# Performance work log

Measured on AMD Instinct MI355X. Metric: run time of the kernel, lower is better.

Reference implementation:

```python
import jax, jax.numpy as jnp
import numpy as np

NB, B, T, D, H = 7, 16, 512, 128, 2
HD = D // H

def _ln(x, s, b):
    m = jnp.mean(x, -1, keepdims=True)
    v = jnp.mean((x - m) ** 2, -1, keepdims=True)
    return (x - m) * jax.lax.rsqrt(v + 1e-5) * s + b

def setup_inputs():
    key = jax.random.key(0)
    keys = iter(jax.random.split(key, 80))
    def w(*shape):
        return jax.random.normal(next(keys), shape, jnp.float32) * 0.02
    inp = {}
    inp['bands'] = jax.random.normal(next(keys), (NB, B, T, D), jnp.float32)
    for nm in ['Wq', 'Wk', 'Wv', 'Wo']:
        inp[nm] = w(NB, D, D)
    for nm in ['bq', 'bk', 'bv', 'bo']:
        inp[nm] = jnp.zeros((NB, D), jnp.float32)
    inp['g_ls'] = jnp.ones((3, D), jnp.float32); inp['g_lb'] = jnp.zeros((3, D), jnp.float32)
    inp['g_w1'] = w(3, D, 2 * D); inp['g_b1'] = jnp.zeros((3, 2 * D), jnp.float32)
    inp['g_w2'] = w(3, 2 * D, D); inp['g_b2'] = jnp.zeros((3, D), jnp.float32)
    inp['g_wg'] = w(3, D, D);     inp['g_bg'] = jnp.zeros((3, D), jnp.float32)
    inp['h_ls'] = jnp.ones((2, D), jnp.float32); inp['h_lb'] = jnp.zeros((2, D), jnp.float32)
    inp['h_w1'] = w(2, D, 3 * D); inp['h_b1'] = jnp.zeros((2, 3 * D), jnp.float32)
    inp['h_w2'] = w(2, 3 * D, D); inp['h_b2'] = jnp.zeros((2, D), jnp.float32)
    inp['r_ls'] = jnp.ones((2, D), jnp.float32); inp['r_lb'] = jnp.zeros((2, D), jnp.float32)
    inp['r_w1'] = w(2, D, 4 * D); inp['r_b1'] = jnp.zeros((2, 4 * D), jnp.float32)
    inp['r_w2'] = w(2, 4 * D, D); inp['r_b2'] = jnp.zeros((2, D), jnp.float32)
    # wormhole: pairs (0,6),(1,5),(2,4) share cross_proj per pair; bridge on band 3
    inp['wp_w'] = w(3, D, D);     inp['wp_b'] = jnp.zeros((3, D), jnp.float32)
    inp['wg_w'] = w(3, 2 * D, D); inp['wg_b'] = jnp.zeros((3, D), jnp.float32)
    inp['br_w'] = w(6, D, D);     inp['br_b'] = jnp.zeros((6, D), jnp.float32)
    inp['bg_w'] = w(2 * D, D);    inp['bg_b'] = jnp.zeros((D,), jnp.float32)
    return inp

def reference(bands, Wq, bq, Wk, bk, Wv, bv, Wo, bo,
              g_ls, g_lb, g_w1, g_b1, g_w2, g_b2, g_wg, g_bg,
              h_ls, h_lb, h_w1, h_b1, h_w2, h_b2,
              r_ls, r_lb, r_w1, r_b1, r_w2, r_b2,
              wp_w, wp_b, wg_w, wg_b, br_w, br_b, bg_w, bg_b):
    n, b, t, d = bands.shape
    # --- per-band causal self-attention, vectorized over the 7 bands ---
    def heads(x):  # [n,b,t,d] -> [n,b,H,t,hd]
        return x.reshape(n, b, t, H, HD).transpose(0, 1, 3, 2, 4)
    q = heads(jnp.einsum('nbtd,nde->nbte', bands, Wq) + bq[:, None, None, :])
    k = heads(jnp.einsum('nbtd,nde->nbte', bands, Wk) + bk[:, None, None, :])
    v = heads(jnp.einsum('nbtd,nde->nbte', bands, Wv) + bv[:, None, None, :])
    scores = jnp.einsum('nbhtd,nbhsd->nbhts', q, k) / np.float32(np.sqrt(HD))
    causal = jnp.triu(jnp.ones((t, t), bool), 1)
    scores = jnp.where(causal, jnp.float32(-1e9), scores)
    attn = jax.nn.softmax(scores, axis=-1)
    o = jnp.einsum('nbhts,nbhsd->nbhtd', attn, v)
    o = o.transpose(0, 1, 3, 2, 4).reshape(n, b, t, d)
    o = jnp.einsum('nbtd,nde->nbte', o, Wo) + bo[:, None, None, :]
    x = bands + o
    # --- band-tier FFN processors ---
    geo, hyb, rea = x[0:3], x[3:5], x[5:7]
    hg = _ln(geo, g_ls[:, None, None, :], g_lb[:, None, None, :])
    hg = jax.nn.gelu(jnp.einsum('nbtd,nde->nbte', hg, g_w1) + g_b1[:, None, None, :], approximate=False)
    hg = jnp.einsum('nbte,ned->nbtd', hg, g_w2) + g_b2[:, None, None, :]
    gate = jax.nn.sigmoid(jnp.einsum('nbtd,nde->nbte', geo, g_wg) + g_bg[:, None, None, :])
    geo = geo + gate * hg
    hh = _ln(hyb, h_ls[:, None, None, :], h_lb[:, None, None, :])
    hh = jax.nn.gelu(jnp.einsum('nbtd,nde->nbte', hh, h_w1) + h_b1[:, None, None, :], approximate=False)
    hyb = hyb + jnp.einsum('nbte,ned->nbtd', hh, h_w2) + h_b2[:, None, None, :]
    hr = _ln(rea, r_ls[:, None, None, :], r_lb[:, None, None, :])
    hr = jax.nn.gelu(jnp.einsum('nbtd,nde->nbte', hr, r_w1) + r_b1[:, None, None, :], approximate=False)
    rea = rea + jnp.einsum('nbte,ned->nbtd', hr, r_w2) + r_b2[:, None, None, :]
    y = jnp.concatenate([geo, hyb, rea], axis=0)
    # --- position-wise wormhole: pairs (0,6),(1,5),(2,4) + bridge band 3 ---
    bl = y[jnp.array([0, 1, 2])]   # low bands of each pair
    bh = y[jnp.array([6, 5, 4])]   # matching high bands
    info_lo = jnp.einsum('nbtd,nde->nbte', bh, wp_w) + wp_b[:, None, None, :]
    info_hi = jnp.einsum('nbtd,nde->nbte', bl, wp_w) + wp_b[:, None, None, :]
    gate_lo = jax.nn.sigmoid(jnp.einsum('nbtd,nde->nbte', jnp.concatenate([bl, info_lo], -1), wg_w) + wg_b[:, None, None, :])
    gate_hi = jax.nn.sigmoid(jnp.einsum('nbtd,nde->nbte', jnp.concatenate([bh, info_hi], -1), wg_w) + wg_b[:, None, None, :])
    out_lo = bl + gate_lo * info_lo
    out_hi = bh + gate_hi * info_hi
    others = y[jnp.array([0, 1, 2, 4, 5, 6])]
    bridge_info = (jnp.einsum('nbtd,nde->bte', others, br_w) + jnp.sum(br_b, 0)) / 6.0
    gate_br = jax.nn.sigmoid(jnp.concatenate([y[3], bridge_info], -1) @ bg_w + bg_b)
    out3 = y[3] + gate_br * bridge_info
    return jnp.stack([out_lo[0], out_lo[1], out_lo[2], out3, out_hi[2], out_hi[1], out_hi[0]], axis=0)
```

## Files before the change

### kernel.cpp

```cpp
#include <hip/hip_runtime.h>
#include <hip/hip_bf16.h>

#define NBAND 7
#define BBATCH 16
#define TSEQ 512
#define DMODEL 128
#define MBAND (BBATCH * TSEQ)
#define BANDE ((size_t)MBAND * DMODEL)

typedef __attribute__((ext_vector_type(8))) short short8;
typedef __attribute__((ext_vector_type(4))) float f32x4;
typedef unsigned int u32;
typedef unsigned short u16;

__device__ __forceinline__ u16 f2bf(float x) {
  unsigned u = __float_as_uint(x);
  unsigned r = u + 0x7FFF + ((u >> 16) & 1);
  return (u16)(r >> 16);
}
__device__ __forceinline__ u32 pack2(float a, float b) {
  return (u32)f2bf(a) | ((u32)f2bf(b) << 16);
}
__device__ __forceinline__ float b2f(u16 h) {
  return __uint_as_float((u32)h << 16);
}

struct TSlice { const float* src; u16* dst; int K, N; };
struct TArgs { TSlice s[62]; };

__global__ __launch_bounds__(256) void wtrans_kernel(TArgs a) {
  TSlice sl = a.s[blockIdx.z];
  const int tk = (blockIdx.x & 7) * 64, tn = (blockIdx.x >> 3) * 64;
  if (tk >= sl.K || tn >= sl.N) return;
  __shared__ __align__(16) u16 T[64][72];
  const int tid = threadIdx.x;
  #pragma unroll
  for (int it = 0; it < 4; ++it) {
    int idx = tid + it * 256;
    int k = idx >> 4, nq = (idx & 15) << 2;
    float4 v = *(const float4*)&sl.src[(size_t)(tk + k) * sl.N + tn + nq];
    T[nq + 0][k] = f2bf(v.x); T[nq + 1][k] = f2bf(v.y);
    T[nq + 2][k] = f2bf(v.z); T[nq + 3][k] = f2bf(v.w);
  }
  __syncthreads();
  #pragma unroll
  for (int it = 0; it < 2; ++it) {
    int idx = tid + it * 256;
    int n = idx >> 3, kq = (idx & 7) << 3;
    *(short8*)&sl.dst[(size_t)(tn + n) * sl.K + tk + kq] = *(const short8*)&T[n][kq];
  }
}

__device__ __forceinline__ void mfma_part_h(const u16* __restrict__ A,
                                            const u16* __restrict__ WT,
                                            int K, int m0, int n0, int tid,
                                            u16 (*As)[40], u16 (*Bs)[40],
                                            f32x4 acc[2][2]) {
  const int lane = tid & 63;
  const int wv = tid >> 6;
  const int wr = wv >> 1, wc = wv & 1;
  const int lr = lane & 15, k8 = lane >> 4;
  const int row = tid >> 2, kq = (tid & 3) << 3;

  const u16* Ar = &A[(size_t)(m0 + row) * K + kq];
  const u16* Br = &WT[(size_t)(n0 + row) * K + kq];
  short8 apre = *(const short8*)Ar;
  short8 bpre = *(const short8*)Br;

  for (int k0 = 0; k0 < K; k0 += 32) {
    __syncthreads();
    *(short8*)&As[row][kq] = apre;
    *(short8*)&Bs[row][kq] = bpre;
    if (k0 + 32 < K) {
      apre = *(const short8*)(Ar + k0 + 32);
      bpre = *(const short8*)(Br + k0 + 32);
    }
    __syncthreads();
    short8 a0 = *(const short8*)&As[wr * 32 + lr][k8 * 8];
    short8 a1 = *(const short8*)&As[wr * 32 + 16 + lr][k8 * 8];
    short8 b0 = *(const short8*)&Bs[wc * 32 + lr][k8 * 8];
    short8 b1 = *(const short8*)&Bs[wc * 32 + 16 + lr][k8 * 8];
    acc[0][0] = __builtin_amdgcn_mfma_f32_16x16x32_bf16(a0, b0, acc[0][0], 0, 0, 0);
    acc[0][1] = __builtin_amdgcn_mfma_f32_16x16x32_bf16(a0, b1, acc[0][1], 0, 0, 0);
    acc[1][0] = __builtin_amdgcn_mfma_f32_16x16x32_bf16(a1, b0, acc[1][0], 0, 0, 0);
    acc[1][1] = __builtin_amdgcn_mfma_f32_16x16x32_bf16(a1, b1, acc[1][1], 0, 0, 0);
  }
}

__device__ __forceinline__ void mfma_part_f(const float* __restrict__ A,
                                            const u16* __restrict__ WT,
                                            int K, int m0, int n0, int tid,
                                            u16 (*As)[40], u16 (*Bs)[40],
                                            f32x4 acc[2][2]) {
  const int lane = tid & 63;
  const int wv = tid >> 6;
  const int wr = wv >> 1, wc = wv & 1;
  const int lr = lane & 15, k8 = lane >> 4;
  const int row = tid >> 2, kq = (tid & 3) << 3;

  const float* Ar = &A[(size_t)(m0 + row) * K + kq];
  const u16* Br = &WT[(size_t)(n0 + row) * K + kq];
  float4 ap0 = *(const float4*)Ar;
  float4 ap1 = *(const float4*)(Ar + 4);
  short8 bpre = *(const short8*)Br;

  for (int k0 = 0; k0 < K; k0 += 32) {
    __syncthreads();
    *(u32*)&As[row][kq]     = pack2(ap0.x, ap0.y);
    *(u32*)&As[row][kq + 2] = pack2(ap0.z, ap0.w);
    *(u32*)&As[row][kq + 4] = pack2(ap1.x, ap1.y);
    *(u32*)&As[row][kq + 6] = pack2(ap1.z, ap1.w);
    *(short8*)&Bs[row][kq] = bpre;
    if (k0 + 32 < K) {
      ap0 = *(const float4*)(Ar + k0 + 32);
      ap1 = *(const float4*)(Ar + k0 + 36);
      bpre = *(const short8*)(Br + k0 + 32);
    }
    __syncthreads();
    short8 a0 = *(const short8*)&As[wr * 32 + lr][k8 * 8];
    short8 a1 = *(const short8*)&As[wr * 32 + 16 + lr][k8 * 8];
    short8 b0 = *(const short8*)&Bs[wc * 32 + lr][k8 * 8];
    short8 b1 = *(const short8*)&Bs[wc * 32 + 16 + lr][k8 * 8];
    acc[0][0] = __builtin_amdgcn_mfma_f32_16x16x32_bf16(a0, b0, acc[0][0], 0, 0, 0);
    acc[0][1] = __builtin_amdgcn_mfma_f32_16x16x32_bf16(a0, b1, acc[0][1], 0, 0, 0);
    acc[1][0] = __builtin_amdgcn_mfma_f32_16x16x32_bf16(a1, b0, acc[1][0], 0, 0, 0);
    acc[1][1] = __builtin_amdgcn_mfma_f32_16x16x32_bf16(a1, b1, acc[1][1], 0, 0, 0);
  }
}

struct ZD {
  const u16 *A, *A2, *WT, *WT2;
  const float* AF;
  const float* bias;
  const float* residF;
  const u16 *residH, *extraH;
  float* OF;
  u16* OH;
  int K, N, op;
  int pad;
};
struct PArgs { ZD z[21]; };

__global__ __launch_bounds__(256) void gemm_b(PArgs p) {
  const ZD d = p.z[blockIdx.z];
  const int n0 = blockIdx.y * 64;
  if (n0 >= d.N) return;
  __shared__ __align__(16) u16 As[64][40];
  __shared__ __align__(16) u16 Bs[64][40];
  const int m0 = blockIdx.x * 64;
  const int tid = threadIdx.x;
  f32x4 acc[2][2] = {};

  if (d.op == 7) {
    const int bl[6] = {0, 1, 2, 4, 5, 6};
    #pragma unroll 1
    for (int s = 0; s < 6; ++s)
      mfma_part_h(d.A + (size_t)bl[s] * BANDE, d.WT + (size_t)s * 16384,
                  128, m0, n0, tid, As, Bs, acc);
  } else {
    if (d.AF) mfma_part_f(d.AF, d.WT, d.K, m0, n0, tid, As, Bs, acc);
    else      mfma_part_h(d.A,  d.WT, d.K, m0, n0, tid, As, Bs, acc);
    if (d.A2)
      mfma_part_h(d.A2, d.WT2, d.K, m0, n0, tid, As, Bs, acc);
  }

  const int lane = tid & 63;
  const int wv = tid >> 6;
  const int wr = wv >> 1, wc = wv & 1;
  const int lr = lane & 15, lg = lane >> 4;

  if (d.op == 6) {
    #pragma unroll
    for (int i = 0; i < 2; ++i) {
      #pragma unroll
      for (int j = 0; j < 2; ++j) {
        int mb = m0 + wr * 32 + i * 16 + lg * 4;
        int n = n0 + wc * 32 + j * 16 + lr;
        float bia = d.bias[n];
        uint2 st;
        st.x = pack2(acc[i][j][0] + bia, acc[i][j][1] + bia);
        st.y = pack2(acc[i][j][2] + bia, acc[i][j][3] + bia);
        *(uint2*)&d.OH[(size_t)n * MBAND + mb] = st;
      }
    }
    return;
  }

  #pragma unroll
  for (int i = 0; i < 2; ++i) {
    #pragma unroll
    for (int j = 0; j < 2; ++j) {
      #pragma unroll
      for (int r = 0; r < 4; ++r) {
        int m = m0 + wr * 32 + i * 16 + lg * 4 + r;
        int n = n0 + wc * 32 + j * 16 + lr;
        float v = acc[i][j][r];
        if (d.bias && d.op != 7) v += d.bias[n];
        size_t idx = (size_t)m * d.N + n;
        switch (d.op) {
          case 0: d.OH[idx] = f2bf(v); break;
          case 1: d.OH[idx] =
                    f2bf(0.5f * v * (1.f + erff(v * 0.70710678118654752f))); break;
          case 2: d.OH[idx] = f2bf(1.f / (1.f + __expf(-v))); break;
          case 3: d.OH[idx] = f2bf(d.residF[idx] + v); break;
          case 4: {
            float gate = 1.f / (1.f + __expf(-v));
            d.OF[idx] = b2f(d.residH[idx]) + gate * b2f(d.extraH[idx]);
          } break;
          case 5: {
            float gm = d.extraH ? b2f(d.extraH[idx]) : 1.f;
            d.OH[idx] = f2bf(b2f(d.residH[idx]) + gm * v);
          } break;
          case 7: {
            float bb = 0.f;
            #pragma unroll
            for (int s = 0; s < 6; ++s) bb += d.bias[s * 128 + n];
            d.OH[idx] = f2bf(v * (1.f / 6.f) + bb * (1.f / 6.f));
          } break;
        }
      }
    }
  }
}

__global__ __launch_bounds__(256) void attn_kernel(const u16* __restrict__ q,
                                                   const u16* __restrict__ k,
                                                   const u16* __restrict__ vT,
                                                   u16* __restrict__ o) {
  const int band = blockIdx.x >> 8;
  const int rest = blockIdx.x & 255;
  const int qt = 7 - (rest & 7);
  const int bh = rest >> 3;
  const int h  = bh & 1;
  const int b  = bh >> 1;
  const size_t rowbase = ((size_t)band * BBATCH + b) * TSEQ;
  const u16* vb = vT + (size_t)band * BANDE + (size_t)h * 64 * MBAND + (size_t)b * TSEQ;

  const int tid  = threadIdx.x;
  const int w    = tid >> 6;
  const int lane = tid & 63;
  const int lr   = lane & 15;
  const int lg   = lane >> 4;

  __shared__ __align__(16) u16 Ks[64][72];
  __shared__ __align__(16) u16 Vs[64][72];
  __shared__ __align__(16) u16 Ps[4][16][72];

  short8 aq[2];
  {
    const u16* qp = &q[(rowbase + qt * 64 + w * 16 + lr) * DMODEL + h * 64 + lg * 8];
    aq[0] = *(const short8*)qp;
    aq[1] = *(const short8*)(qp + 32);
  }

  short8 kpre[2], vpre[2];
  #pragma unroll
  for (int it = 0; it < 2; ++it) {
    int idx = tid + it * 256;
    int r = idx >> 3, c8 = (idx & 7) << 3;
    kpre[it] = *(const short8*)&k[(rowbase + r) * DMODEL + h * 64 + c8];
    vpre[it] = *(const short8*)&vb[(size_t)r * MBAND + c8];
  }

  f32x4 oacc[4] = {};
  float m[4], l[4];
  #pragma unroll
  for (int r = 0; r < 4; ++r) { m[r] = -1e30f; l[r] = 0.f; }

  for (int kt = 0; kt <= qt; ++kt) {
    __syncthreads();
    #pragma unroll
    for (int it = 0; it < 2; ++it) {
      int idx = tid + it * 256;
      int r = idx >> 3, c8 = (idx & 7) << 3;
      *(short8*)&Ks[r][c8] = kpre[it];
      *(short8*)&Vs[r][c8] = vpre[it];
    }
    if (kt < qt) {
      int nt = kt + 1;
      #pragma unroll
      for (int it = 0; it < 2; ++it) {
        int idx = tid + it * 256;
        int r = idx >> 3, c8 = (idx & 7) << 3;
        kpre[it] = *(const short8*)&k[(rowbase + nt * 64 + r) * DMODEL + h * 64 + c8];
        vpre[it] = *(const short8*)&vb[(size_t)r * MBAND + nt * 64 + c8];
      }
    }
    __syncthreads();

    f32x4 s[4] = {};
    #pragma unroll
    for (int c = 0; c < 2; ++c) {
      short8 a = aq[c];
      #pragma unroll
      for (int j = 0; j < 4; ++j) {
        short8 bb = *(const short8*)&Ks[j * 16 + lr][c * 32 + lg * 8];
        s[j] = __builtin_amdgcn_mfma_f32_16x16x32_bf16(a, bb, s[j], 0, 0, 0);
      }
    }
    #pragma unroll
    for (int j = 0; j < 4; ++j)
      #pragma unroll
      for (int r = 0; r < 4; ++r)
        s[j][r] *= 0.125f;

    if (kt == qt) {
      #pragma unroll
      for (int j = 0; j < 4; ++j)
        #pragma unroll
        for (int r = 0; r < 4; ++r) {
          int row = w * 16 + lg * 4 + r;
          int col = j * 16 + lr;
          if (col > row) s[j][r] = -1e30f;
        }
    }

    float mx[4], al[4];
    #pragma unroll
    for (int r = 0; r < 4; ++r)
      mx[r] = fmaxf(fmaxf(s[0][r], s[1][r]), fmaxf(s[2][r], s[3][r]));
    #pragma unroll
    for (int off = 1; off <= 8; off <<= 1)
      #pragma unroll
      for (int r = 0; r < 4; ++r)
        mx[r] = fmaxf(mx[r], __shfl_xor(mx[r], off));
    #pragma unroll
    for (int r = 0; r < 4; ++r) {
      float mn = fmaxf(m[r], mx[r]);
      al[r] = __expf(m[r] - mn);
      m[r] = mn;
    }
    float rs[4] = {0.f, 0.f, 0.f, 0.f};
    #pragma unroll
    for (int j = 0; j < 4; ++j)
      #pragma unroll
      for (int r = 0; r < 4; ++r) {
        float pe = __expf(s[j][r] - m[r]);
        s[j][r] = pe;
        rs[r] += pe;
      }
    #pragma unroll
    for (int off = 1; off <= 8; off <<= 1)
      #pragma unroll
      for (int r = 0; r < 4; ++r)
        rs[r] += __shfl_xor(rs[r], off);
    #pragma unroll
    for (int r = 0; r < 4; ++r) l[r] = l[r] * al[r] + rs[r];

    #pragma unroll
    for (int j = 0; j < 4; ++j)
      #pragma unroll
      for (int r = 0; r < 4; ++r)
        oacc[j][r] *= al[r];

    #pragma unroll
    for (int j = 0; j < 4; ++j)
      #pragma unroll
      for (int r = 0; r < 4; ++r)
        Ps[w][lg * 4 + r][j * 16 + lr] = f2bf(s[j][r]);

    #pragma unroll
    for (int c = 0; c < 2; ++c) {
      short8 a = *(const short8*)&Ps[w][lr][c * 32 + lg * 8];
      #pragma unroll
      for (int j = 0; j < 4; ++j) {
        short8 bb = *(const short8*)&Vs[j * 16 + lr][c * 32 + lg * 8];
        oacc[j] = __builtin_amdgcn_mfma_f32_16x16x32_bf16(a, bb, oacc[j], 0, 0, 0);
      }
    }
  }

  float inv[4];
  #pragma unroll
  for (int r = 0; r < 4; ++r) inv[r] = 1.f / l[r];
  #pragma unroll
  for (int j = 0; j < 4; ++j)
    #pragma unroll
    for (int r = 0; r < 4; ++r) {
      size_t row = rowbase + qt * 64 + w * 16 + lg * 4 + r;
      o[row * DMODEL + h * 64 + j * 16 + lr] = f2bf(oacc[j][r] * inv[r]);
    }
}

struct LNA {
  const u16* x;
  u16* xn;
  const float* ls[7];
  const float* lb[7];
};

__global__ __launch_bounds__(256) void ln_kernel(LNA p) {
  const int tid = threadIdx.x;
  const int rr = tid >> 6, lane = tid & 63;
  const size_t row = (size_t)blockIdx.x * 4 + rr;
  u32 wv = *(const u32*)&p.x[row * DMODEL + 2 * lane];
  float a = b2f((u16)wv), b = b2f((u16)(wv >> 16));
  float s = a + b;
  #pragma unroll
  for (int off = 32; off; off >>= 1) s += __shfl_xor(s, off);
  float mean = s * (1.f / 128.f);
  float da = a - mean, db = b - mean;
  float vs = da * da + db * db;
  #pragma unroll
  for (int off = 32; off; off >>= 1) vs += __shfl_xor(vs, off);
  float rstd = rsqrtf(vs * (1.f / 128.f) + 1e-5f);
  int band = (int)(row >> 13);
  const float* ls = p.ls[band];
  const float* lb = p.lb[band];
  *(u32*)&p.xn[row * DMODEL + 2 * lane] =
      pack2(da * rstd * ls[2 * lane] + lb[2 * lane],
            db * rstd * ls[2 * lane + 1] + lb[2 * lane + 1]);
}

extern "C" void kernel_launch(void* const* d_in, const int* in_sizes, int n_in,
                              void* d_out, int out_size, void* d_ws, size_t ws_size,
                              hipStream_t stream) {
  bool dict = (in_sizes[2] != 896);
  const float* bands = (const float*)d_in[0];
  const float* Wq = (const float*)d_in[1];
  const float *Wk, *Wv, *Wo, *bq, *bk, *bv, *bo;
  if (dict) {
    Wk = (const float*)d_in[2]; Wv = (const float*)d_in[3]; Wo = (const float*)d_in[4];
    bq = (const float*)d_in[5]; bk = (const float*)d_in[6];
    bv = (const float*)d_in[7]; bo = (const float*)d_in[8];
  } else {
    bq = (const float*)d_in[2]; Wk = (const float*)d_in[3]; bk = (const float*)d_in[4];
    Wv = (const float*)d_in[5]; bv = (const float*)d_in[6];
    Wo = (const float*)d_in[7]; bo = (const float*)d_in[8];
  }
  const float* g_ls = (const float*)d_in[9];
  const float* g_lb = (const float*)d_in[10];
  const float* g_w1 = (const float*)d_in[11];
  const float* g_b1 = (const float*)d_in[12];
  const float* g_w2 = (const float*)d_in[13];
  const float* g_b2 = (const float*)d_in[14];
  const float* g_wg = (const float*)d_in[15];
  const float* g_bg = (const float*)d_in[16];
  const float* h_ls = (const float*)d_in[17];
  const float* h_lb = (const float*)d_in[18];
  const float* h_w1 = (const float*)d_in[19];
  const float* h_b1 = (const float*)d_in[20];
  const float* h_w2 = (const float*)d_in[21];
  const float* h_b2 = (const float*)d_in[22];
  const float* r_ls = (const float*)d_in[23];
  const float* r_lb = (const float*)d_in[24];
  const float* r_w1 = (const float*)d_in[25];
  const float* r_b1 = (const float*)d_in[26];
  const float* r_w2 = (const float*)d_in[27];
  const float* r_b2 = (const float*)d_in[28];
  const float* wp_w = (const float*)d_in[29];
  const float* wp_b = (const float*)d_in[30];
  const float* wg_w = (const float*)d_in[31];
  const float* wg_b = (const float*)d_in[32];
  const float* br_w = (const float*)d_in[33];
  const float* br_b = (const float*)d_in[34];
  const float* bg_w = (const float*)d_in[35];
  const float* bg_b = (const float*)d_in[36];
  float* out = (float*)d_out;

  const float* lsP[7] = {g_ls, g_ls + 128, g_ls + 256, h_ls, h_ls + 128, r_ls, r_ls + 128};
  const float* lbP[7] = {g_lb, g_lb + 128, g_lb + 256, h_lb, h_lb + 128, r_lb, r_lb + 128};
  const float* b1p[7] = {g_b1, g_b1 + 256, g_b1 + 512,
                         h_b1, h_b1 + 384, r_b1, r_b1 + 512};
  const float* b2p[7] = {g_b2, g_b2 + 128, g_b2 + 256,
                         h_b2, h_b2 + 128, r_b2, r_b2 + 128};
  const int hN[7] = {256, 256, 256, 384, 384, 512, 512};

  const size_t HIDSZ = (size_t)MBAND * 2560;
  u16* H = (u16*)d_ws;
  u16* hidh = H;
  u16* qh = H + HIDSZ;
  u16* kh = qh + 7 * BANDE;
  u16* vh = kh + 7 * BANDE;
  u16* oh = vh + 7 * BANDE;
  u16* wt = oh + 7 * BANDE;
  u16* wtQ   = wt;
  u16* wtK   = wtQ + 7 * 16384;
  u16* wtV   = wtK + 7 * 16384;
  u16* wtO   = wtV + 7 * 16384;
  u16* wtGwg = wtO + 7 * 16384;
  u16* wtWp  = wtGwg + 3 * 16384;
  u16* wtBr  = wtWp + 3 * 16384;
  u16* wtWg  = wtBr + 6 * 16384;
  u16* wtBg  = wtWg + 6 * 16384;
  u16* wtG1  = wtBg + 2 * 16384;
  u16* wtH1  = wtG1 + 3 * 32768;
  u16* wtR1  = wtH1 + 2 * 49152;
  u16* wtG2  = wtR1 + 2 * 65536;
  u16* wtH2  = wtG2 + 3 * 32768;
  u16* wtR2  = wtH2 + 2 * 49152;
  u16* xh = qh;
  u16* xnh = kh;
  u16* gateh = vh;
  u16* yh = oh;
  u16* infoh = hidh;
  u16* bridgeh = hidh + 6 * BANDE;

  size_t hOff[7];
  {
    size_t acc = 0;
    for (int n = 0; n < 7; ++n) { hOff[n] = acc; acc += (size_t)MBAND * hN[n]; }
  }
  u16* wtW1s[7] = {wtG1, wtG1 + 32768, wtG1 + 65536,
                   wtH1, wtH1 + 49152, wtR1, wtR1 + 65536};
  u16* wtW2s[7] = {wtG2, wtG2 + 32768, wtG2 + 65536,
                   wtH2, wtH2 + 49152, wtR2, wtR2 + 65536};

  auto LP = [&](PArgs& p, int Z, int ymax) {
    dim3 grid(MBAND / 64, ymax, Z);
    gemm_b<<<grid, dim3(256), 0, stream>>>(p);
  };

  {
    TArgs ta{};
    int ns = 0;
    auto add = [&](const float* s, u16* d, int K, int N) {
      ta.s[ns].src = s; ta.s[ns].dst = d; ta.s[ns].K = K; ta.s[ns].N = N; ++ns;
    };
    for (int z = 0; z < 7; ++z) add(Wq + z * 16384, wtQ + z * 16384, 128, 128);
    for (int z = 0; z < 7; ++z) add(Wk + z * 16384, wtK + z * 16384, 128, 128);
    for (int z = 0; z < 7; ++z) add(Wv + z * 16384, wtV + z * 16384, 128, 128);
    for (int z = 0; z < 7; ++z) add(Wo + z * 16384, wtO + z * 16384, 128, 128);
    for (int i = 0; i < 3; ++i) add(g_wg + i * 16384, wtGwg + i * 16384, 128, 128);
    for (int i = 0; i < 3; ++i) add(wp_w + i * 16384, wtWp + i * 16384, 128, 128);
    for (int j = 0; j < 6; ++j) add(br_w + j * 16384, wtBr + j * 16384, 128, 128);
    for (int i = 0; i < 3; ++i) {
      add(wg_w + i * 32768,         wtWg + (size_t)(2 * i) * 16384,     128, 128);
      add(wg_w + i * 32768 + 16384, wtWg + (size_t)(2 * i + 1) * 16384, 128, 128);
    }
    add(bg_w,         wtBg,         128, 128);
    add(bg_w + 16384, wtBg + 16384, 128, 128);
    for (int i = 0; i < 3; ++i) add(g_w1 + i * 32768, wtG1 + i * 32768, 128, 256);
    for (int i = 0; i < 2; ++i) add(h_w1 + i * 49152, wtH1 + i * 49152, 128, 384);
    for (int i = 0; i < 2; ++i) add(r_w1 + i * 65536, wtR1 + i * 65536, 128, 512);
    for (int i = 0; i < 3; ++i) add(g_w2 + i * 32768, wtG2 + i * 32768, 256, 128);
    for (int i = 0; i < 2; ++i) add(h_w2 + i * 49152, wtH2 + i * 49152, 384, 128);
    for (int i = 0; i < 2; ++i) add(r_w2 + i * 65536, wtR2 + i * 65536, 512, 128);
    wtrans_kernel<<<dim3(64, 1, 62), dim3(256), 0, stream>>>(ta);
  }

  {
    PArgs p{};
    const u16* wtQKV[3] = {wtQ, wtK, wtV};
    const float* bqkv[3] = {bq, bk, bv};
    u16* oqkv[3] = {qh, kh, vh};
    for (int w = 0; w < 3; ++w)
      for (int band = 0; band < 7; ++band) {
        ZD& d = p.z[w * 7 + band];
        d.AF = bands + (size_t)band * BANDE;
        d.WT = wtQKV[w] + (size_t)band * 16384;
        d.bias = bqkv[w] + band * 128;
        d.OH = oqkv[w] + (size_t)band * BANDE;
        d.K = 128; d.N = 128; d.op = (w == 2) ? 6 : 0;
      }
    LP(p, 21, 2);
  }

  attn_kernel<<<dim3(NBAND * 256), dim3(256), 0, stream>>>(qh, kh, vh, oh);

  {
    PArgs p{};
    for (int band = 0; band < 7; ++band) {
      ZD& d = p.z[band];
      d.A = oh + (size_t)band * BANDE;
      d.WT = wtO + (size_t)band * 16384;
      d.bias = bo + band * 128;
      d.residF = bands + (size_t)band * BANDE;
      d.OH = xh + (size_t)band * BANDE;
      d.K = 128; d.N = 128; d.op = 3;
    }
    LP(p, 7, 2);
  }

  {
    LNA p{};
    p.x = xh; p.xn = xnh;
    for (int n = 0; n < 7; ++n) { p.ls[n] = lsP[n]; p.lb[n] = lbP[n]; }
    ln_kernel<<<dim3(NBAND * MBAND / 4), dim3(256), 0, stream>>>(p);
  }

  {
    PArgs p{};
    for (int z = 0; z < 3; ++z) {
      ZD& d = p.z[z];
      d.A = xh + (size_t)z * BANDE;
      d.WT = wtGwg + (size_t)z * 16384;
      d.bias = g_bg + z * 128;
      d.OH = gateh + (size_t)z * BANDE;
      d.K = 128; d.N = 128; d.op = 2;
    }
    for (int band = 0; band < 7; ++band) {
      ZD& d = p.z[3 + band];
      d.A = xnh + (size_t)band * BANDE;
      d.WT = wtW1s[band];
      d.bias = b1p[band];
      d.OH = hidh + hOff[band];
      d.K = 128; d.N = hN[band]; d.op = 1;
    }
    LP(p, 10, 8);
  }

  {
    PArgs p{};
    for (int band = 0; band < 7; ++band) {
      ZD& d = p.z[band];
      d.A = hidh + hOff[band];
      d.WT = wtW2s[band];
      d.bias = b2p[band];
      d.residH = xh + (size_t)band * BANDE;
      d.extraH = (band < 3) ? gateh + (size_t)band * BANDE : nullptr;
      d.OH = yh + (size_t)band * BANDE;
      d.K = hN[band]; d.N = 128; d.op = 5;
    }
    LP(p, 7, 2);
  }

  {
    PArgs p{};
    for (int z = 0; z < 6; ++z) {
      int t = (z < 3) ? z : z + 1;
      int src = 6 - t;
      int i = (t < 3) ? t : 6 - t;
      ZD& d = p.z[z];
      d.A = yh + (size_t)src * BANDE;
      d.WT = wtWp + (size_t)i * 16384;
      d.bias = wp_b + i * 128;
      d.OH = infoh + (size_t)z * BANDE;
      d.K = 128; d.N = 128; d.op = 0;
    }
    {
      ZD& d = p.z[6];
      d.A = yh;
      d.WT = wtBr;
      d.bias = br_b;
      d.OH = bridgeh;
      d.K = 128; d.N = 128; d.op = 7;
    }
    LP(p, 7, 2);
  }

  {
    PArgs p{};
    for (int z = 0; z < 6; ++z) {
      int t = (z < 3) ? z : z + 1;
      int i = (t < 3) ? t : 6 - t;
      ZD& d = p.z[z];
      d.A = yh + (size_t)t * BANDE;
      d.WT = wtWg + (size_t)(2 * i) * 16384;
      d.A2 = infoh + (size_t)z * BANDE;
      d.WT2 = wtWg + (size_t)(2 * i + 1) * 16384;
      d.bias = wg_b + i * 128;
      d.residH = yh + (size_t)t * BANDE;
      d.extraH = infoh + (size_t)z * BANDE;
      d.OF = out + (size_t)t * BANDE;
      d.K = 128; d.N = 128; d.op = 4;
    }
    {
      ZD& d = p.z[6];
      d.A = yh + 3 * BANDE;
      d.WT = wtBg;
      d.A2 = bridgeh;
      d.WT2 = wtBg + 16384;
      d.bias = bg_b;
      d.residH = yh + 3 * BANDE;
      d.extraH = bridgeh;
      d.OF = out + 3 * BANDE;
      d.K = 128; d.N = 128; d.op = 4;
    }
    LP(p, 7, 2);
  }
}
```

Baseline: 220.4 us.

## Pair causal query tiles per block to balance attention work and share K/V loads

The attention kernel now launches 512-thread blocks, each handling two query tiles (qt = 7-p and qt = p) with four waves apiece. Every block then does a fixed eight tiles of causal work, and the two tiles share each K/V tile staged in shared memory. This removes the load imbalance of triangular causal blocks and halves redundant K/V loads. In exchange, the waves on the shorter tile sit idle at barriers during later iterations, and the larger blocks may lower occupancy.

```diff
diff --git a/kernel.cpp b/kernel.cpp
--- a/kernel.cpp
+++ b/kernel.cpp
@@ -223,16 +223,15 @@
   }
 }
 
-__global__ __launch_bounds__(256) void attn_kernel(const u16* __restrict__ q,
+__global__ __launch_bounds__(512) void attn_kernel(const u16* __restrict__ q,
                                                    const u16* __restrict__ k,
                                                    const u16* __restrict__ vT,
                                                    u16* __restrict__ o) {
-  const int band = blockIdx.x >> 8;
-  const int rest = blockIdx.x & 255;
-  const int qt = 7 - (rest & 7);
-  const int bh = rest >> 3;
-  const int h  = bh & 1;
-  const int b  = bh >> 1;
+  const int bx   = blockIdx.x;
+  const int pp   = bx & 3;
+  const int h    = (bx >> 2) & 1;
+  const int b    = (bx >> 3) & 15;
+  const int band = bx >> 7;
   const size_t rowbase = ((size_t)band * BBATCH + b) * TSEQ;
   const u16* vb = vT + (size_t)band * BANDE + (size_t)h * 64 * MBAND + (size_t)b * TSEQ;
 
@@ -242,130 +241,121 @@
   const int lr   = lane & 15;
   const int lg   = lane >> 4;
 
+  const int qtA = 7 - pp;
+  const int qt_w = (w < 4) ? qtA : pp;
+  const int wr4 = w & 3;
+
   __shared__ __align__(16) u16 Ks[64][72];
   __shared__ __align__(16) u16 Vs[64][72];
-  __shared__ __align__(16) u16 Ps[4][16][72];
+  __shared__ __align__(16) u16 Ps[8][16][72];
 
   short8 aq[2];
   {
-    const u16* qp = &q[(rowbase + qt * 64 + w * 16 + lr) * DMODEL + h * 64 + lg * 8];
+    const u16* qp = &q[(rowbase + qt_w * 64 + wr4 * 16 + lr) * DMODEL + h * 64 + lg * 8];
     aq[0] = *(const short8*)qp;
     aq[1] = *(const short8*)(qp + 32);
   }
 
-  short8 kpre[2], vpre[2];
-  #pragma unroll
-  for (int it = 0; it < 2; ++it) {
-    int idx = tid + it * 256;
-    int r = idx >> 3, c8 = (idx & 7) << 3;
-    kpre[it] = *(const short8*)&k[(rowbase + r) * DMODEL + h * 64 + c8];
-    vpre[it] = *(const short8*)&vb[(size_t)r * MBAND + c8];
-  }
+  const int sr = tid >> 3, sc8 = (tid & 7) << 3;
+  short8 kpre = *(const short8*)&k[(rowbase + sr) * DMODEL + h * 64 + sc8];
+  short8 vpre = *(const short8*)&vb[(size_t)sr * MBAND + sc8];
 
   f32x4 oacc[4] = {};
   float m[4], l[4];
   #pragma unroll
   for (int r = 0; r < 4; ++r) { m[r] = -1e30f; l[r] = 0.f; }
 
-  for (int kt = 0; kt <= qt; ++kt) {
+  for (int kt = 0; kt <= qtA; ++kt) {
     __syncthreads();
-    #pragma unroll
-    for (int it = 0; it < 2; ++it) {
-      int idx = tid + it * 256;
-      int r = idx >> 3, c8 = (idx & 7) << 3;
-      *(short8*)&Ks[r][c8] = kpre[it];
-      *(short8*)&Vs[r][c8] = vpre[it];
-    }
-    if (kt < qt) {
+    *(short8*)&Ks[sr][sc8] = kpre;
+    *(short8*)&Vs[sr][sc8] = vpre;
+    if (kt < qtA) {
       int nt = kt + 1;
-      #pragma unroll
-      for (int it = 0; it < 2; ++it) {
-        int idx = tid + it * 256;
-        int r = idx >> 3, c8 = (idx & 7) << 3;
-        kpre[it] = *(const short8*)&k[(rowbase + nt * 64 + r) * DMODEL + h * 64 + c8];
-        vpre[it] = *(const short8*)&vb[(size_t)r * MBAND + nt * 64 + c8];
+      kpre = *(const short8*)&k[(rowbase + nt * 64 + sr) * DMODEL + h * 64 + sc8];
+      vpre = *(const short8*)&vb[(size_t)sr * MBAND + nt * 64 + sc8];
+    }
+    __syncthreads();
+
+    if (kt <= qt_w) {
+      f32x4 s[4] = {};
+      #pragma unroll
+      for (int c = 0; c < 2; ++c) {
+        short8 a = aq[c];
+        #pragma unroll
+        for (int j = 0; j < 4; ++j) {
+          short8 bb = *(const short8*)&Ks[j * 16 + lr][c * 32 + lg * 8];
+          s[j] = __builtin_amdgcn_mfma_f32_16x16x32_bf16(a, bb, s[j], 0, 0, 0);
+        }
       }
-    }
-    __syncthreads();
-
-    f32x4 s[4] = {};
-    #pragma unroll
-    for (int c = 0; c < 2; ++c) {
-      short8 a = aq[c];
-      #pragma unroll
-      for (int j = 0; j < 4; ++j) {
-        short8 bb = *(const short8*)&Ks[j * 16 + lr][c * 32 + lg * 8];
-        s[j] = __builtin_amdgcn_mfma_f32_16x16x32_bf16(a, bb, s[j], 0, 0, 0);
+      #pragma unroll
+      for (int j = 0; j < 4; ++j)
+        #pragma unroll
+        for (int r = 0; r < 4; ++r)
+          s[j][r] *= 0.125f;
+
+      if (kt == qt_w) {
+        #pragma unroll
+        for (int j = 0; j < 4; ++j)
+          #pragma unroll
+          for (int r = 0; r < 4; ++r) {
+            int row = wr4 * 16 + lg * 4 + r;
+            int col = j * 16 + lr;
+            if (col > row) s[j][r] = -1e30f;
+          }
       }
-    }
-    #pragma unroll
-    for (int j = 0; j < 4; ++j)
+
+      float mx[4], al[4];
       #pragma unroll
       for (int r = 0; r < 4; ++r)
-        s[j][r] *= 0.125f;
-
-    if (kt == qt) {
+        mx[r] = fmaxf(fmaxf(s[0][r], s[1][r]), fmaxf(s[2][r], s[3][r]));
+      #pragma unroll
+      for (int off = 1; off <= 8; off <<= 1)
+        #pragma unroll
+        for (int r = 0; r < 4; ++r)
+          mx[r] = fmaxf(mx[r], __shfl_xor(mx[r], off));
+      #pragma unroll
+      for (int r = 0; r < 4; ++r) {
+        float mn = fmaxf(m[r], mx[r]);
+        al[r] = __expf(m[r] - mn);
+        m[r] = mn;
+      }
+      float rs[4] = {0.f, 0.f, 0.f, 0.f};
       #pragma unroll
       for (int j = 0; j < 4; ++j)
         #pragma unroll
         for (int r = 0; r < 4; ++r) {
-          int row = w * 16 + lg * 4 + r;
-          int col = j * 16 + lr;
-          if (col > row) s[j][r] = -1e30f;
+          float pe = __expf(s[j][r] - m[r]);
+          s[j][r] = pe;
+          rs[r] += pe;
         }
-    }
-
-    float mx[4], al[4];
-    #pragma unroll
-    for (int r = 0; r < 4; ++r)
-      mx[r] = fmaxf(fmaxf(s[0][r], s[1][r]), fmaxf(s[2][r], s[3][r]));
-    #pragma unroll
-    for (int off = 1; off <= 8; off <<= 1)
-      #pragma unroll
-      for (int r = 0; r < 4; ++r)
-        mx[r] = fmaxf(mx[r], __shfl_xor(mx[r], off));
-    #pragma unroll
-    for (int r = 0; r < 4; ++r) {
-      float mn = fmaxf(m[r], mx[r]);
-      al[r] = __expf(m[r] - mn);
-      m[r] = mn;
-    }
-    float rs[4] = {0.f, 0.f, 0.f, 0.f};
-    #pragma unroll
-    for (int j = 0; j < 4; ++j)
-      #pragma unroll
-      for (int r = 0; r < 4; ++r) {
-        float pe = __expf(s[j][r] - m[r]);
-        s[j][r] = pe;
-        rs[r] += pe;
-      }
-    #pragma unroll
-    for (int off = 1; off <= 8; off <<= 1)
-      #pragma unroll
-      for (int r = 0; r < 4; ++r)
-        rs[r] += __shfl_xor(rs[r], off);
-    #pragma unroll
-    for (int r = 0; r < 4; ++r) l[r] = l[r] * al[r] + rs[r];
-
-    #pragma unroll
-    for (int j = 0; j < 4; ++j)
-      #pragma unroll
-      for (int r = 0; r < 4; ++r)
-        oacc[j][r] *= al[r];
-
-    #pragma unroll
-    for (int j = 0; j < 4; ++j)
-      #pragma unroll
-      for (int r = 0; r < 4; ++r)
-        Ps[w][lg * 4 + r][j * 16 + lr] = f2bf(s[j][r]);
-
-    #pragma unroll
-    for (int c = 0; c < 2; ++c) {
-      short8 a = *(const short8*)&Ps[w][lr][c * 32 + lg * 8];
-      #pragma unroll
-      for (int j = 0; j < 4; ++j) {
-        short8 bb = *(const short8*)&Vs[j * 16 + lr][c * 32 + lg * 8];
-        oacc[j] = __builtin_amdgcn_mfma_f32_16x16x32_bf16(a, bb, oacc[j], 0, 0, 0);
+      #pragma unroll
+      for (int off = 1; off <= 8; off <<= 1)
+        #pragma unroll
+        for (int r = 0; r < 4; ++r)
+          rs[r] += __shfl_xor(rs[r], off);
+      #pragma unroll
+      for (int r = 0; r < 4; ++r) l[r] = l[r] * al[r] + rs[r];
+
+      #pragma unroll
+      for (int j = 0; j < 4; ++j)
+        #pragma unroll
+        for (int r = 0; r < 4; ++r)
+          oacc[j][r] *= al[r];
+
+      #pragma unroll
+      for (int j = 0; j < 4; ++j)
+        #pragma unroll
+        for (int r = 0; r < 4; ++r)
+          Ps[w][lg * 4 + r][j * 16 + lr] = f2bf(s[j][r]);
+
+      #pragma unroll
+      for (int c = 0; c < 2; ++c) {
+        short8 a = *(const short8*)&Ps[w][lr][c * 32 + lg * 8];
+        #pragma unroll
+        for (int j = 0; j < 4; ++j) {
+          short8 bb = *(const short8*)&Vs[j * 16 + lr][c * 32 + lg * 8];
+          oacc[j] = __builtin_amdgcn_mfma_f32_16x16x32_bf16(a, bb, oacc[j], 0, 0, 0);
+        }
       }
     }
   }
@@ -377,7 +367,7 @@
   for (int j = 0; j < 4; ++j)
     #pragma unroll
     for (int r = 0; r < 4; ++r) {
-      size_t row = rowbase + qt * 64 + w * 16 + lg * 4 + r;
+      size_t row = rowbase + qt_w * 64 + wr4 * 16 + lg * 4 + r;
       o[row * DMODEL + h * 64 + j * 16 + lr] = f2bf(oacc[j][r] * inv[r]);
     }
 }
@@ -556,7 +546,7 @@
     LP(p, 21, 2);
   }
 
-  attn_kernel<<<dim3(NBAND * 256), dim3(256), 0, stream>>>(qh, kh, vh, oh);
+  attn_kernel<<<dim3(NBAND * BBATCH * 2 * 4), dim3(512), 0, stream>>>(qh, kh, vh, oh);
 
   {
     PArgs p{};
```

New measurement: 208.0 us (median of 2 runs). 5.7% less time.
